# Kernel optimization log

Hardware: AMD Instinct MI355X
Metric: run time of the kernel (lower is better)

The kernel has to match this reference:

```python
import jax, jax.numpy as jnp
import numpy as np
from jax import lax

CHUNK = 256
ROPE_BASE = 10000.0


def setup_inputs() -> dict:
    D, H, K = 2048, 16, 4
    Dh = D // H
    key = jax.random.key(0)
    ks = jax.random.split(key, 8)
    x = jax.random.normal(ks[0], (2, 4096, D), dtype=jnp.float32)
    norm_scale = jnp.ones((D,), jnp.float32)
    conv_w = jax.random.normal(ks[1], (D, 1, K), jnp.float32) * 0.1
    conv_b = jnp.zeros((D,), jnp.float32)
    in_proj_w = jax.random.normal(ks[2], (3 * D, D), jnp.float32) * 0.02
    out_proj_w = jax.random.normal(ks[3], (D, D), jnp.float32) * 0.02
    # dt_bias init as in torch module
    u = jax.random.uniform(ks[4], (H, Dh), jnp.float32)
    dt = jnp.clip(jnp.exp(u * (np.log(0.1) - np.log(10.0)) + np.log(10.0)), 0.001, None)
    dt_bias = (dt + jnp.log(-jnp.expm1(-dt))).reshape(-1)
    head_mix = jnp.eye(H, dtype=jnp.float32)
    return {"x": x, "norm_scale": norm_scale, "conv_w": conv_w, "conv_b": conv_b,
            "in_proj_w": in_proj_w, "dt_bias": dt_bias, "head_mix": head_mix,
            "out_proj_w": out_proj_w}


def _forward(x, norm_scale, conv_w, conv_b, in_proj_w, dt_bias, head_mix, out_proj_w):
    B, N, D = x.shape
    H = head_mix.shape[0]
    Dh = D // H
    K = conv_w.shape[-1]
    residual = x
    # RMSNorm (fp32 with clamp)
    xf = x.astype(jnp.float32)
    rms = lax.rsqrt(jnp.mean(xf * xf, -1, keepdims=True) + 1e-6)
    xn = jnp.clip(norm_scale * xf * rms, -60000.0, 60000.0).astype(x.dtype)
    # causal depthwise conv1d (torch pads K-1 then truncates to N)
    xc = lax.conv_general_dilated(xn.transpose(0, 2, 1), conv_w, (1,), [(K - 1, 0)],
                                  dimension_numbers=("NCH", "OIH", "NCH"),
                                  feature_group_count=D)
    xc = xc + conv_b[None, :, None]
    xc = jax.nn.silu(xc.transpose(0, 2, 1))  # (B,N,D)
    fused = xc @ in_proj_w.T  # (B,N,3D)
    dt_raw, v, gate = jnp.split(fused, 3, axis=-1)
    dt = jnp.clip(jax.nn.softplus(dt_raw.astype(jnp.float32) + dt_bias), 0.001, 2.0)
    gate = jax.nn.sigmoid(gate)
    log_alpha = -dt  # (B,N,D) fp32
    # RoPE on v per head
    inv_freq = 1.0 / (ROPE_BASE ** (jnp.arange(0, Dh, 2, dtype=jnp.float32) / Dh))
    t = jnp.arange(N, dtype=jnp.float32)
    freqs = t[:, None] * inv_freq[None, :]  # (N, Dh//2)
    cos = jnp.cos(freqs)[None, :, None, :]
    sin = jnp.sin(freqs)[None, :, None, :]
    v4 = v.reshape(B, N, H, Dh)
    v1, v2 = v4[..., : Dh // 2], v4[..., Dh // 2:]
    v_rot = jnp.concatenate([v1 * cos - v2 * sin, v1 * sin + v2 * cos], -1).reshape(B, N, D)
    v_in = v_rot * dt  # fp32
    # pad to chunk multiple (static)
    pad = (-N) % CHUNK
    if pad:
        v_in = jnp.pad(v_in, ((0, 0), (0, pad), (0, 0)))
        log_alpha = jnp.pad(log_alpha, ((0, 0), (0, pad), (0, 0)))
    NC = v_in.shape[1] // CHUNK
    vc = v_in.reshape(B, NC, CHUNK, D)
    la = log_alpha.reshape(B, NC, CHUNK, D)
    # intra-chunk stabilized scan
    L = jnp.clip(jnp.cumsum(la, axis=2), -20.0, 0.0)
    Lmax = jnp.max(L, axis=2, keepdims=True)
    Ls = L - Lmax
    cum = jnp.cumsum(jnp.exp(-Ls) * vc, axis=2)
    chunk_out = jnp.exp(Ls) * cum
    if NC > 1:
        bd = L[:, :, -1, :]             # (B,NC,D) boundary decay
        bo = chunk_out[:, :, -1, :]     # boundary out
        cd = jnp.clip(jnp.cumsum(bd, axis=1), -80.0, 0.0)
        stab = jnp.max(cd, axis=1, keepdims=True)
        ncd = jnp.clip(cd - stab, -20.0, 0.0)
        seeds = bo * jnp.exp(-ncd)
        shifted = jnp.pad(seeds[:, :-1], ((0, 0), (1, 0), (0, 0)))
        carries = jnp.cumsum(shifted, axis=1) * jnp.exp(ncd)
        final = chunk_out + carries[:, :, None, :] * jnp.exp(L)
    else:
        final = chunk_out
    final = final.astype(x.dtype).reshape(B, -1, D)[:, :N, :]
    # head mixing
    vm = jnp.einsum("bnhd,hm->bnmd", final.reshape(B, N, H, Dh), head_mix).reshape(B, N, D)
    out = (vm * gate) @ out_proj_w.T
    return residual + out


def reference(x, norm_scale, conv_w, conv_b, in_proj_w, dt_bias, head_mix, out_proj_w):
    return _forward(x, norm_scale, conv_w, conv_b, in_proj_w, dt_bias, head_mix, out_proj_w)
```

## Files before the change

kernel.cpp:

```cpp
#include <hip/hip_runtime.h>
#include <hip/hip_bf16.h>
#include <math.h>

#define B_ 2
#define N_ 4096
#define D_ 2048
#define H_ 16
#define DH_ 128
#define CHUNK_ 256
#define NC_ 16
#define M_ (B_*N_)
#define F3D (3*D_)

typedef __bf16 v8bf __attribute__((ext_vector_type(8)));
typedef float  v4f  __attribute__((ext_vector_type(4)));
typedef unsigned short u16x8 __attribute__((ext_vector_type(8)));

__device__ __forceinline__ float bf2f(unsigned short u) {
    union { unsigned int i; float f; } c; c.i = ((unsigned int)u) << 16; return c.f;
}
__device__ __forceinline__ unsigned short f2bf(float f) {
    __hip_bfloat16 h = __float2bfloat16(f);
    return *(unsigned short*)&h;
}

__device__ __forceinline__ void async_copy16(void* lds, const void* g) {
    __builtin_amdgcn_global_load_lds(
        (const __attribute__((address_space(1))) unsigned int*)g,
        (__attribute__((address_space(3))) unsigned int*)lds,
        16, 0, 0);
}

__global__ __launch_bounds__(256) void k_rmsnorm(const float* __restrict__ x,
                                                 const float* __restrict__ scale,
                                                 __hip_bfloat16* __restrict__ xn)
{
    __shared__ float red[4];
    const int row = blockIdx.x;
    const float4* x4 = (const float4*)(x + (size_t)row * D_);
    float4 a = x4[threadIdx.x*2];
    float4 b = x4[threadIdx.x*2 + 1];
    float ss = a.x*a.x + a.y*a.y + a.z*a.z + a.w*a.w
             + b.x*b.x + b.y*b.y + b.z*b.z + b.w*b.w;
    #pragma unroll
    for (int off = 32; off > 0; off >>= 1) ss += __shfl_down(ss, off, 64);
    if ((threadIdx.x & 63) == 0) red[threadIdx.x >> 6] = ss;
    __syncthreads();
    float tot = red[0] + red[1] + red[2] + red[3];
    float r = rsqrtf(tot / (float)D_ + 1e-6f);
    const float4* s4 = (const float4*)scale;
    float4 sa = s4[threadIdx.x*2];
    float4 sb = s4[threadIdx.x*2 + 1];
    float v[8] = { sa.x*a.x, sa.y*a.y, sa.z*a.z, sa.w*a.w,
                   sb.x*b.x, sb.y*b.y, sb.z*b.z, sb.w*b.w };
    u16x8 o;
    #pragma unroll
    for (int j = 0; j < 8; ++j) {
        float t = fminf(fmaxf(v[j]*r, -60000.f), 60000.f);
        o[j] = f2bf(t);
    }
    ((u16x8*)(xn + (size_t)row * D_))[threadIdx.x] = o;
}

__global__ __launch_bounds__(256) void k_conv_silu(const __hip_bfloat16* __restrict__ xn,
                                                   const float* __restrict__ w,
                                                   const float* __restrict__ bias,
                                                   __hip_bfloat16* __restrict__ xc)
{
    size_t p = (size_t)blockIdx.x * 256 + threadIdx.x;
    size_t e0 = p * 8;
    int d0 = (int)(e0 & (D_-1));
    int n  = (int)((e0 >> 11) & (N_-1));
    const float4* w4 = (const float4*)w;
    float acc[8];
    const float4* b4 = (const float4*)(bias + d0);
    float4 ba = b4[0], bb = b4[1];
    acc[0]=ba.x; acc[1]=ba.y; acc[2]=ba.z; acc[3]=ba.w;
    acc[4]=bb.x; acc[5]=bb.y; acc[6]=bb.z; acc[7]=bb.w;
    float4 wv[8];
    #pragma unroll
    for (int j = 0; j < 8; ++j) wv[j] = w4[d0 + j];
    #pragma unroll
    for (int k = 0; k < 4; ++k) {
        int nn = n - 3 + k;
        if (nn >= 0) {
            u16x8 t = *(const u16x8*)(xn + e0 - (size_t)(3-k)*D_);
            #pragma unroll
            for (int j = 0; j < 8; ++j) {
                float wk = (k==0)?wv[j].x:(k==1)?wv[j].y:(k==2)?wv[j].z:wv[j].w;
                acc[j] += bf2f(t[j]) * wk;
            }
        }
    }
    u16x8 o;
    #pragma unroll
    for (int j = 0; j < 8; ++j) {
        float s = acc[j] / (1.f + __expf(-acc[j]));
        o[j] = f2bf(s);
    }
    *(u16x8*)(xc + e0) = o;
}

__global__ __launch_bounds__(256) void k_cast_bf16(const float* __restrict__ src,
                                                   __hip_bfloat16* __restrict__ dst)
{
    size_t p = (size_t)blockIdx.x * 256 + threadIdx.x;
    const float4* s4 = (const float4*)src;
    float4 a = s4[p*2], b = s4[p*2 + 1];
    u16x8 o;
    o[0]=f2bf(a.x); o[1]=f2bf(a.y); o[2]=f2bf(a.z); o[3]=f2bf(a.w);
    o[4]=f2bf(b.x); o[5]=f2bf(b.y); o[6]=f2bf(b.z); o[7]=f2bf(b.w);
    ((u16x8*)dst)[p] = o;
}

template<int MODE>
__global__ __launch_bounds__(256, 3) void k_gemm(const __hip_bfloat16* __restrict__ Abf,
                                              const __hip_bfloat16* __restrict__ Wbf,
                                              int K,
                                              float* __restrict__ o0,
                                              __hip_bfloat16* __restrict__ o1,
                                              __hip_bfloat16* __restrict__ o2,
                                              const float* __restrict__ dt_bias,
                                              const float* __restrict__ resid,
                                              float* __restrict__ outp)
{
    __shared__ __attribute__((aligned(16))) char lds[3][2][8192];
    const __bf16* A = (const __bf16*)Abf;
    const __bf16* W = (const __bf16*)Wbf;
    const int tid  = threadIdx.x;
    const int wave = tid >> 6;
    const int lane = tid & 63;

    const int bx = blockIdx.x;
    const int by = blockIdx.y;

    const size_t m0 = (size_t)bx * 128;
    const size_t n0 = (size_t)by * 128;
    const int wm = (wave & 1) * 64;
    const int wn = (wave >> 1) * 64;

    v4f acc[4][4] = {};

    const int fr = lane & 15;
    const int qk = lane >> 4;
    const int srL = lane >> 3;
    const int ssL = lane & 7;

    const int nt = K >> 5;

    auto stage = [&](int T, int isB) {
        char* reg = &lds[T % 3][isB][0];
        const __bf16* gp = (isB ? W + n0 * (size_t)K : A + m0 * (size_t)K);
        #pragma unroll
        for (int is = 0; is < 2; ++is) {
            int r  = is*32 + wave*8 + srL;
            int u  = ssL ^ (r & 7);
            int m  = 2*r + (u >> 2);
            int kg = u & 3;
            const __bf16* src = gp + (size_t)m * K + (T << 5) + kg*8;
            async_copy16((void*)(reg + is*4096 + wave*1024), (const void*)src);
        }
    };
    auto rd = [&](v8bf* f, const char* reg, int wbase) {
        #pragma unroll
        for (int i = 0; i < 4; ++i) {
            int m = wbase + i*16 + fr;
            int r = m >> 1;
            int s = (((m & 1) << 2) | qk) ^ (r & 7);
            f[i] = *(const v8bf*)(reg + r*128 + s*16);
        }
    };

    stage(0, 0); stage(0, 1);
    stage(1, 0); stage(1, 1);

    for (int t = 0; t < nt; ++t) {
        if (t + 1 < nt) { asm volatile("s_waitcnt vmcnt(4)" ::: "memory"); }
        else            { asm volatile("s_waitcnt vmcnt(0)" ::: "memory"); }
        __builtin_amdgcn_s_barrier();
        __builtin_amdgcn_sched_barrier(0);

        const char* Ab = &lds[t % 3][0][0];
        const char* Bb = &lds[t % 3][1][0];

        if (t + 2 < nt) { stage(t + 2, 0); stage(t + 2, 1); }

        v8bf fa[4], fb[4];
        rd(fa, Ab, wm);
        rd(fb, Bb, wn);

        __builtin_amdgcn_s_setprio(1);
        #pragma unroll
        for (int i = 0; i < 4; ++i)
            #pragma unroll
            for (int j = 0; j < 4; ++j)
                acc[i][j] = __builtin_amdgcn_mfma_f32_16x16x32_bf16(fa[i], fb[j], acc[i][j], 0, 0, 0);
        __builtin_amdgcn_s_setprio(0);
    }

    const int col = lane & 15;
    const int rb  = (lane >> 4) * 4;
    if (MODE == 0) {
        const int stream = by >> 4;
        const size_t nb = n0 - (size_t)stream * D_;
        #pragma unroll
        for (int i = 0; i < 4; ++i)
            #pragma unroll
            for (int j = 0; j < 4; ++j) {
                size_t nIdx = nb + wn + j*16 + col;
                #pragma unroll
                for (int r = 0; r < 4; ++r) {
                    size_t m = m0 + wm + i*16 + rb + r;
                    size_t off = m * (size_t)D_ + nIdx;
                    float v = acc[i][j][r];
                    if (stream == 0) {
                        float xx = v + dt_bias[nIdx];
                        float e  = __expf(-fabsf(xx));
                        float sp = fmaxf(xx, 0.f) + __logf(1.f + e);
                        float dt = fminf(fmaxf(sp, 0.001f), 2.0f);
                        o0[off] = -dt;
                    } else if (stream == 1) {
                        o1[off] = __float2bfloat16(v);
                    } else {
                        o2[off] = __float2bfloat16(1.f/(1.f+__expf(-v)));
                    }
                }
            }
    } else {
        #pragma unroll
        for (int i = 0; i < 4; ++i)
            #pragma unroll
            for (int j = 0; j < 4; ++j)
                #pragma unroll
                for (int r = 0; r < 4; ++r) {
                    size_t m = m0 + wm + i*16 + rb + r;
                    size_t off = m * (size_t)D_ + n0 + wn + j*16 + col;
                    outp[off] = acc[i][j][r] + resid[off];
                }
    }
}

__global__ __launch_bounds__(256) void k_scan1(const float* __restrict__ la,
                                               const __hip_bfloat16* __restrict__ v,
                                               float* __restrict__ bd, float* __restrict__ bo,
                                               float* __restrict__ nc,
                                               __hip_bfloat16* __restrict__ expL)
{
    int idx = blockIdx.x * 256 + threadIdx.x;
    int d = idx & (D_-1);
    int c = (idx >> 11) & (NC_-1);
    int b = idx >> 15;
    int i = d & 63;
    const bool firstHalf = (d & 64) == 0;
    float inv = __expf((float)i * (-9.210340371976184f / 64.f));
    int n0 = c * CHUNK_;
    float cs = cosf((float)n0 * inv), sn = sinf((float)n0 * inv);
    float ca = cosf(inv), sa = sinf(inv);
    size_t row0 = (size_t)b * N_ + (size_t)c * CHUNK_;
    float S = 0.f, Lp = 0.f, out = 0.f;
    #pragma unroll 8
    for (int t = 0; t < CHUNK_; ++t) {
        size_t off = (row0 + t) * (size_t)D_ + d;
        float a  = la[off];
        float vo = __bfloat162float(v[off]);
        float vp = __bfloat162float(v[firstHalf ? off + 64 : off - 64]);
        float dt = -a;
        float vin = (firstHalf ? (vo*cs - vp*sn) : (vp*sn + vo*cs)) * dt;
        S += a;
        float L = fmaxf(S, -20.f);
        out = __expf(L - Lp) * out + vin;
        Lp = L;
        nc[off]   = out;
        expL[off] = __float2bfloat16(__expf(L));
        float csn = cs*ca - sn*sa;
        sn = sn*ca + cs*sa;
        cs = csn;
    }
    bd[idx] = Lp;
    bo[idx] = out;
}

__global__ __launch_bounds__(256) void k_scan2(const float* __restrict__ bd,
                                               const float* __restrict__ bo,
                                               float* __restrict__ carries)
{
    int idx = blockIdx.x * 256 + threadIdx.x;
    int d = idx & (D_-1);
    int b = idx >> 11;
    float bd0 = bd[(size_t)(b*NC_)*D_ + d];
    float cd = 0.f, acc = 0.f;
    #pragma unroll
    for (int c = 0; c < NC_; ++c) {
        size_t o = (size_t)(b*NC_ + c)*D_ + d;
        cd = fmaxf(cd + bd[o], -80.f);
        float ncd = fmaxf(cd - bd0, -20.f);
        carries[o] = acc * __expf(ncd);
        acc += bo[o] * __expf(-ncd);
    }
}

__global__ __launch_bounds__(256) void k_scanfix(const float* __restrict__ nc,
                                                 __hip_bfloat16* __restrict__ stex,
                                                 const float* __restrict__ carr)
{
    size_t idx = (size_t)blockIdx.x * 256 + threadIdx.x;
    size_t e0 = idx * 8;
    int d0 = (int)(e0 & (D_-1));
    int token = (int)(e0 >> 11);
    int b = token >> 12;
    int c = (token & (N_-1)) >> 8;
    const float* cp = carr + ((size_t)(b*NC_ + c)) * D_ + d0;
    u16x8 el = ((const u16x8*)stex)[idx];
    const float4* n4 = (const float4*)(nc + e0);
    float4 na = n4[0], nb = n4[1];
    const float4* c4 = (const float4*)cp;
    float4 ca = c4[0], cb = c4[1];
    float nv[8] = { na.x, na.y, na.z, na.w, nb.x, nb.y, nb.z, nb.w };
    float cv[8] = { ca.x, ca.y, ca.z, ca.w, cb.x, cb.y, cb.z, cb.w };
    u16x8 o;
    #pragma unroll
    for (int j = 0; j < 8; ++j)
        o[j] = f2bf(nv[j] + cv[j] * bf2f(el[j]));
    ((u16x8*)stex)[idx] = o;
}

__global__ __launch_bounds__(256) void k_headmix_gate(const __hip_bfloat16* __restrict__ state,
                                                      const __hip_bfloat16* __restrict__ gate,
                                                      const float* __restrict__ hm,
                                                      __hip_bfloat16* __restrict__ y)
{
    __shared__ float lf[D_];
    __shared__ float lhm[H_*H_];
    const int row = blockIdx.x;
    const size_t base = (size_t)row * D_;
    u16x8 s8 = ((const u16x8*)(state + base))[threadIdx.x];
    #pragma unroll
    for (int j = 0; j < 8; ++j) lf[threadIdx.x*8 + j] = bf2f(s8[j]);
    if (threadIdx.x < H_*H_) lhm[threadIdx.x] = hm[threadIdx.x];
    __syncthreads();
    #pragma unroll
    for (int k = 0; k < 8; ++k) {
        int o = threadIdx.x + k*256;
        int m  = o >> 7;
        int dh = o & 127;
        float s = 0.f;
        #pragma unroll
        for (int h = 0; h < H_; ++h) s += lf[h*DH_ + dh] * lhm[h*H_ + m];
        float g = __bfloat162float(gate[base + o]);
        y[base + o] = __float2bfloat16(s * g);
    }
}

extern "C" void kernel_launch(void* const* d_in, const int* in_sizes, int n_in,
                              void* d_out, int out_size, void* d_ws, size_t ws_size,
                              hipStream_t stream)
{
    const float* x          = (const float*)d_in[0];
    const float* norm_scale = (const float*)d_in[1];
    const float* conv_w     = (const float*)d_in[2];
    const float* conv_b     = (const float*)d_in[3];
    const float* in_proj_w  = (const float*)d_in[4];
    const float* dt_bias    = (const float*)d_in[5];
    const float* head_mix   = (const float*)d_in[6];
    const float* out_proj_w = (const float*)d_in[7];
    float* out = (float*)d_out;

    char* ws = (char*)d_ws;
    float*          la   = (float*)ws;
    __hip_bfloat16* xn   = (__hip_bfloat16*)(ws + 67108864);
    __hip_bfloat16* xc   = (__hip_bfloat16*)(ws + 100663296);
    __hip_bfloat16* gate = (__hip_bfloat16*)(ws + 134217728);
    __hip_bfloat16* w2   = (__hip_bfloat16*)(ws + 167772160);
    float*          bd   = (float*)(ws + 176160768);
    float*          bo   = (float*)(ws + 176422912);
    float*          carr = (float*)(ws + 176685056);
    __hip_bfloat16* w1   = xn;
    float*          nc   = (float*)(ws + 67108864);
    __hip_bfloat16* y    = xc;
    __hip_bfloat16* v     = (__hip_bfloat16*)d_out;
    __hip_bfloat16* stex  = (__hip_bfloat16*)((char*)d_out + 33554432);

    k_rmsnorm<<<M_, 256, 0, stream>>>(x, norm_scale, xn);
    k_conv_silu<<<(M_*(size_t)D_)/8/256, 256, 0, stream>>>(xn, conv_w, conv_b, xc);
    k_cast_bf16<<<6144, 256, 0, stream>>>(in_proj_w, w1);
    k_cast_bf16<<<2048, 256, 0, stream>>>(out_proj_w, w2);
    k_gemm<0><<<dim3(M_/128, F3D/128), 256, 0, stream>>>(xc, w1, D_, la, v, gate, dt_bias, nullptr, nullptr);
    k_scan1<<<(B_*NC_*D_)/256, 256, 0, stream>>>(la, v, bd, bo, nc, stex);
    k_scan2<<<(B_*D_)/256, 256, 0, stream>>>(bd, bo, carr);
    k_scanfix<<<(M_*(size_t)D_)/8/256, 256, 0, stream>>>(nc, stex, carr);
    k_headmix_gate<<<M_, 256, 0, stream>>>(stex, gate, head_mix, y);
    k_gemm<1><<<dim3(M_/128, D_/128), 256, 0, stream>>>(y, w2, D_, nullptr, nullptr, nullptr, nullptr, x, out);
}
```

Before: 688.3 us.

## Fuse scan fixup into head-mix, store log-decay in bf16, restructure GEMM pipeline

```diff
diff --git a/kernel.cpp b/kernel.cpp
--- a/kernel.cpp
+++ b/kernel.cpp
@@ -101,41 +101,42 @@
     *(u16x8*)(xc + e0) = o;
 }
 
-__global__ __launch_bounds__(256) void k_cast_bf16(const float* __restrict__ src,
-                                                   __hip_bfloat16* __restrict__ dst)
+#define W1_VECS 1572864
+__global__ __launch_bounds__(256) void k_cast2(const float* __restrict__ s1,
+                                               __hip_bfloat16* __restrict__ d1,
+                                               const float* __restrict__ s2,
+                                               __hip_bfloat16* __restrict__ d2)
 {
     size_t p = (size_t)blockIdx.x * 256 + threadIdx.x;
+    const float* src; __hip_bfloat16* dst; size_t q;
+    if (p < W1_VECS) { src = s1; dst = d1; q = p; }
+    else             { src = s2; dst = d2; q = p - W1_VECS; }
     const float4* s4 = (const float4*)src;
-    float4 a = s4[p*2], b = s4[p*2 + 1];
+    float4 a = s4[q*2], b = s4[q*2 + 1];
     u16x8 o;
     o[0]=f2bf(a.x); o[1]=f2bf(a.y); o[2]=f2bf(a.z); o[3]=f2bf(a.w);
     o[4]=f2bf(b.x); o[5]=f2bf(b.y); o[6]=f2bf(b.z); o[7]=f2bf(b.w);
-    ((u16x8*)dst)[p] = o;
+    ((u16x8*)dst)[q] = o;
 }
 
 template<int MODE>
-__global__ __launch_bounds__(256, 3) void k_gemm(const __hip_bfloat16* __restrict__ Abf,
+__global__ __launch_bounds__(256, 4) void k_gemm(const __hip_bfloat16* __restrict__ Abf,
                                               const __hip_bfloat16* __restrict__ Wbf,
-                                              int K,
-                                              float* __restrict__ o0,
+                                              __hip_bfloat16* __restrict__ o0,
                                               __hip_bfloat16* __restrict__ o1,
                                               __hip_bfloat16* __restrict__ o2,
                                               const float* __restrict__ dt_bias,
                                               const float* __restrict__ resid,
                                               float* __restrict__ outp)
 {
-    __shared__ __attribute__((aligned(16))) char lds[3][2][8192];
+    __shared__ __attribute__((aligned(16))) char lds[2][2][8192];
     const __bf16* A = (const __bf16*)Abf;
     const __bf16* W = (const __bf16*)Wbf;
     const int tid  = threadIdx.x;
     const int wave = tid >> 6;
     const int lane = tid & 63;
-
-    const int bx = blockIdx.x;
-    const int by = blockIdx.y;
-
-    const size_t m0 = (size_t)bx * 128;
-    const size_t n0 = (size_t)by * 128;
+    const size_t m0 = (size_t)blockIdx.x * 128;
+    const size_t n0 = (size_t)blockIdx.y * 128;
     const int wm = (wave & 1) * 64;
     const int wn = (wave >> 1) * 64;
 
@@ -143,65 +144,79 @@
 
     const int fr = lane & 15;
     const int qk = lane >> 4;
-    const int srL = lane >> 3;
-    const int ssL = lane & 7;
-
-    const int nt = K >> 5;
-
-    auto stage = [&](int T, int isB) {
-        char* reg = &lds[T % 3][isB][0];
-        const __bf16* gp = (isB ? W + n0 * (size_t)K : A + m0 * (size_t)K);
-        #pragma unroll
-        for (int is = 0; is < 2; ++is) {
-            int r  = is*32 + wave*8 + srL;
-            int u  = ssL ^ (r & 7);
-            int m  = 2*r + (u >> 2);
-            int kg = u & 3;
-            const __bf16* src = gp + (size_t)m * K + (T << 5) + kg*8;
-            async_copy16((void*)(reg + is*4096 + wave*1024), (const void*)src);
-        }
-    };
-    auto rd = [&](v8bf* f, const char* reg, int wbase) {
-        #pragma unroll
-        for (int i = 0; i < 4; ++i) {
-            int m = wbase + i*16 + fr;
-            int r = m >> 1;
-            int s = (((m & 1) << 2) | qk) ^ (r & 7);
-            f[i] = *(const v8bf*)(reg + r*128 + s*16);
-        }
-    };
-
-    stage(0, 0); stage(0, 1);
-    stage(1, 0); stage(1, 1);
-
-    for (int t = 0; t < nt; ++t) {
-        if (t + 1 < nt) { asm volatile("s_waitcnt vmcnt(4)" ::: "memory"); }
-        else            { asm volatile("s_waitcnt vmcnt(0)" ::: "memory"); }
+    int mA = wm + fr, rA = mA >> 1;
+    int mB = wn + fr, rB = mB >> 1;
+    const char* vA = &lds[0][0][0] + rA*128 + (((((mA&1)<<2)|qk) ^ (rA&7)) << 4);
+    const char* vB = &lds[0][1][0] + rB*128 + (((((mB&1)<<2)|qk) ^ (rB&7)) << 4);
+
+    const int srL = lane >> 3, ssL = lane & 7;
+    const __bf16 *sA0, *sA1, *sB0, *sB1;
+    {
+        int r0 = wave*8 + srL,      u0 = ssL ^ (r0 & 7);
+        int r1 = 32 + wave*8 + srL, u1 = ssL ^ (r1 & 7);
+        int ma0 = 2*r0 + (u0 >> 2), kg0 = u0 & 3;
+        int ma1 = 2*r1 + (u1 >> 2), kg1 = u1 & 3;
+        sA0 = A + (m0 + ma0)*(size_t)2048 + kg0*8;
+        sA1 = A + (m0 + ma1)*(size_t)2048 + kg1*8;
+        sB0 = W + (n0 + ma0)*(size_t)2048 + kg0*8;
+        sB1 = W + (n0 + ma1)*(size_t)2048 + kg1*8;
+    }
+    char* dA0 = &lds[0][0][0] + wave*1024;
+    char* dB0 = &lds[0][1][0] + wave*1024;
+
+    #define STAGE(BUF) do { \
+        async_copy16(dA0 + (BUF)*16384,        sA0); \
+        async_copy16(dA0 + (BUF)*16384 + 4096, sA1); \
+        async_copy16(dB0 + (BUF)*16384,        sB0); \
+        async_copy16(dB0 + (BUF)*16384 + 4096, sB1); \
+        sA0 += 32; sA1 += 32; sB0 += 32; sB1 += 32; } while(0)
+
+    STAGE(0);
+
+    for (int i2 = 0; i2 < 32; ++i2) {
+        asm volatile("s_waitcnt vmcnt(0)" ::: "memory");
         __builtin_amdgcn_s_barrier();
         __builtin_amdgcn_sched_barrier(0);
-
-        const char* Ab = &lds[t % 3][0][0];
-        const char* Bb = &lds[t % 3][1][0];
-
-        if (t + 2 < nt) { stage(t + 2, 0); stage(t + 2, 1); }
-
-        v8bf fa[4], fb[4];
-        rd(fa, Ab, wm);
-        rd(fb, Bb, wn);
-
-        __builtin_amdgcn_s_setprio(1);
-        #pragma unroll
-        for (int i = 0; i < 4; ++i)
-            #pragma unroll
-            for (int j = 0; j < 4; ++j)
-                acc[i][j] = __builtin_amdgcn_mfma_f32_16x16x32_bf16(fa[i], fb[j], acc[i][j], 0, 0, 0);
-        __builtin_amdgcn_s_setprio(0);
-    }
+        STAGE(1);
+        {
+            v8bf fa[4], fb[4];
+            #pragma unroll
+            for (int i = 0; i < 4; ++i) fa[i] = *(const v8bf*)(vA + i*1024);
+            #pragma unroll
+            for (int j = 0; j < 4; ++j) fb[j] = *(const v8bf*)(vB + j*1024);
+            __builtin_amdgcn_s_setprio(1);
+            #pragma unroll
+            for (int i = 0; i < 4; ++i)
+                #pragma unroll
+                for (int j = 0; j < 4; ++j)
+                    acc[i][j] = __builtin_amdgcn_mfma_f32_16x16x32_bf16(fa[i], fb[j], acc[i][j], 0, 0, 0);
+            __builtin_amdgcn_s_setprio(0);
+        }
+        asm volatile("s_waitcnt vmcnt(0)" ::: "memory");
+        __builtin_amdgcn_s_barrier();
+        __builtin_amdgcn_sched_barrier(0);
+        if (i2 + 1 < 32) STAGE(0);
+        {
+            v8bf fa[4], fb[4];
+            #pragma unroll
+            for (int i = 0; i < 4; ++i) fa[i] = *(const v8bf*)(vA + 16384 + i*1024);
+            #pragma unroll
+            for (int j = 0; j < 4; ++j) fb[j] = *(const v8bf*)(vB + 16384 + j*1024);
+            __builtin_amdgcn_s_setprio(1);
+            #pragma unroll
+            for (int i = 0; i < 4; ++i)
+                #pragma unroll
+                for (int j = 0; j < 4; ++j)
+                    acc[i][j] = __builtin_amdgcn_mfma_f32_16x16x32_bf16(fa[i], fb[j], acc[i][j], 0, 0, 0);
+            __builtin_amdgcn_s_setprio(0);
+        }
+    }
+    #undef STAGE
 
     const int col = lane & 15;
     const int rb  = (lane >> 4) * 4;
     if (MODE == 0) {
-        const int stream = by >> 4;
+        const int stream = blockIdx.y >> 4;
         const size_t nb = n0 - (size_t)stream * D_;
         #pragma unroll
         for (int i = 0; i < 4; ++i)
@@ -218,7 +233,7 @@
                         float e  = __expf(-fabsf(xx));
                         float sp = fmaxf(xx, 0.f) + __logf(1.f + e);
                         float dt = fminf(fmaxf(sp, 0.001f), 2.0f);
-                        o0[off] = -dt;
+                        o0[off] = __float2bfloat16(-dt);
                     } else if (stream == 1) {
                         o1[off] = __float2bfloat16(v);
                     } else {
@@ -240,7 +255,7 @@
     }
 }
 
-__global__ __launch_bounds__(256) void k_scan1(const float* __restrict__ la,
+__global__ __launch_bounds__(256) void k_scan1(const __hip_bfloat16* __restrict__ la,
                                                const __hip_bfloat16* __restrict__ v,
                                                float* __restrict__ bd, float* __restrict__ bo,
                                                float* __restrict__ nc,
@@ -261,7 +276,7 @@
     #pragma unroll 8
     for (int t = 0; t < CHUNK_; ++t) {
         size_t off = (row0 + t) * (size_t)D_ + d;
-        float a  = la[off];
+        float a  = __bfloat162float(la[off]);
         float vo = __bfloat162float(v[off]);
         float vp = __bfloat162float(v[firstHalf ? off + 64 : off - 64]);
         float dt = -a;
@@ -299,44 +314,31 @@
     }
 }
 
-__global__ __launch_bounds__(256) void k_scanfix(const float* __restrict__ nc,
-                                                 __hip_bfloat16* __restrict__ stex,
-                                                 const float* __restrict__ carr)
-{
-    size_t idx = (size_t)blockIdx.x * 256 + threadIdx.x;
-    size_t e0 = idx * 8;
-    int d0 = (int)(e0 & (D_-1));
-    int token = (int)(e0 >> 11);
-    int b = token >> 12;
-    int c = (token & (N_-1)) >> 8;
-    const float* cp = carr + ((size_t)(b*NC_ + c)) * D_ + d0;
-    u16x8 el = ((const u16x8*)stex)[idx];
-    const float4* n4 = (const float4*)(nc + e0);
+__global__ __launch_bounds__(256) void k_hmix(const float* __restrict__ nc,
+                                              const __hip_bfloat16* __restrict__ expL,
+                                              const float* __restrict__ carr,
+                                              const __hip_bfloat16* __restrict__ gate,
+                                              const float* __restrict__ hm,
+                                              __hip_bfloat16* __restrict__ y)
+{
+    __shared__ float lf[D_];
+    __shared__ float lhm[H_*H_];
+    const int row = blockIdx.x;
+    const size_t base = (size_t)row * D_;
+    const int b = row >> 12;
+    const int c = (row >> 8) & (NC_-1);
+    const float* cp = carr + ((size_t)(b*NC_ + c)) * D_ + threadIdx.x*8;
+    u16x8 el = ((const u16x8*)(expL + base))[threadIdx.x];
+    const float4* n4 = (const float4*)(nc + base + threadIdx.x*8);
     float4 na = n4[0], nb = n4[1];
     const float4* c4 = (const float4*)cp;
     float4 ca = c4[0], cb = c4[1];
     float nv[8] = { na.x, na.y, na.z, na.w, nb.x, nb.y, nb.z, nb.w };
     float cv[8] = { ca.x, ca.y, ca.z, ca.w, cb.x, cb.y, cb.z, cb.w };
-    u16x8 o;
     #pragma unroll
     for (int j = 0; j < 8; ++j)
-        o[j] = f2bf(nv[j] + cv[j] * bf2f(el[j]));
-    ((u16x8*)stex)[idx] = o;
-}
-
-__global__ __launch_bounds__(256) void k_headmix_gate(const __hip_bfloat16* __restrict__ state,
-                                                      const __hip_bfloat16* __restrict__ gate,
-                                                      const float* __restrict__ hm,
-                                                      __hip_bfloat16* __restrict__ y)
-{
-    __shared__ float lf[D_];
-    __shared__ float lhm[H_*H_];
-    const int row = blockIdx.x;
-    const size_t base = (size_t)row * D_;
-    u16x8 s8 = ((const u16x8*)(state + base))[threadIdx.x];
-    #pragma unroll
-    for (int j = 0; j < 8; ++j) lf[threadIdx.x*8 + j] = bf2f(s8[j]);
-    if (threadIdx.x < H_*H_) lhm[threadIdx.x] = hm[threadIdx.x];
+        lf[threadIdx.x*8 + j] = nv[j] + cv[j] * bf2f(el[j]);
+    lhm[threadIdx.x] = hm[threadIdx.x];
     __syncthreads();
     #pragma unroll
     for (int k = 0; k < 8; ++k) {
@@ -366,7 +368,7 @@
     float* out = (float*)d_out;
 
     char* ws = (char*)d_ws;
-    float*          la   = (float*)ws;
+    __hip_bfloat16* la   = (__hip_bfloat16*)ws;
     __hip_bfloat16* xn   = (__hip_bfloat16*)(ws + 67108864);
     __hip_bfloat16* xc   = (__hip_bfloat16*)(ws + 100663296);
     __hip_bfloat16* gate = (__hip_bfloat16*)(ws + 134217728);
@@ -376,18 +378,16 @@
     float*          carr = (float*)(ws + 176685056);
     __hip_bfloat16* w1   = xn;
     float*          nc   = (float*)(ws + 67108864);
-    __hip_bfloat16* y    = xc;
+    __hip_bfloat16* y    = (__hip_bfloat16*)ws;
     __hip_bfloat16* v     = (__hip_bfloat16*)d_out;
     __hip_bfloat16* stex  = (__hip_bfloat16*)((char*)d_out + 33554432);
 
     k_rmsnorm<<<M_, 256, 0, stream>>>(x, norm_scale, xn);
     k_conv_silu<<<(M_*(size_t)D_)/8/256, 256, 0, stream>>>(xn, conv_w, conv_b, xc);
-    k_cast_bf16<<<6144, 256, 0, stream>>>(in_proj_w, w1);
-    k_cast_bf16<<<2048, 256, 0, stream>>>(out_proj_w, w2);
-    k_gemm<0><<<dim3(M_/128, F3D/128), 256, 0, stream>>>(xc, w1, D_, la, v, gate, dt_bias, nullptr, nullptr);
+    k_cast2<<<8192, 256, 0, stream>>>(in_proj_w, w1, out_proj_w, w2);
+    k_gemm<0><<<dim3(M_/128, F3D/128), 256, 0, stream>>>(xc, w1, la, v, gate, dt_bias, nullptr, nullptr);
     k_scan1<<<(B_*NC_*D_)/256, 256, 0, stream>>>(la, v, bd, bo, nc, stex);
     k_scan2<<<(B_*D_)/256, 256, 0, stream>>>(bd, bo, carr);
-    k_scanfix<<<(M_*(size_t)D_)/8/256, 256, 0, stream>>>(nc, stex, carr);
-    k_headmix_gate<<<M_, 256, 0, stream>>>(stex, gate, head_mix, y);
-    k_gemm<1><<<dim3(M_/128, D_/128), 256, 0, stream>>>(y, w2, D_, nullptr, nullptr, nullptr, nullptr, x, out);
-}
+    k_hmix<<<M_, 256, 0, stream>>>(nc, stex, carr, gate, head_mix, y);
+    k_gemm<1><<<dim3(M_/128, D_/128), 256, 0, stream>>>(y, w2, nullptr, nullptr, nullptr, nullptr, x, out);
+}
```

Measured after the change: 637.1 us. 7.4% less time.
